# Kernel optimization log

Hardware: AMD Instinct MI355X
Metric: run time of the kernel (lower is better)

Reference implementation:

```python
import jax, jax.numpy as jnp
import numpy as np

SEQ, BATCH, HIDDEN = 2048, 2, 1024
NUM_HEADS, HEAD_DIM = 16, 64
LN_EPS = 1e-6
NEG_INF = -1e10


def setup_inputs() -> dict:
    key = jax.random.key(0)
    k1, k2, k3, k4 = jax.random.split(key, 4)
    inputs_q = jax.random.normal(k1, (SEQ, BATCH, HIDDEN), dtype=jnp.float32)
    # mask convention (TE flax): True / 1 => position is masked out
    mask = jax.random.randint(k2, (BATCH, 1, SEQ, SEQ), 0, 2).astype(bool)
    ln_scale = jnp.ones((HIDDEN,), dtype=jnp.float32)
    ln_bias = jnp.zeros((HIDDEN,), dtype=jnp.float32)
    # fused QKV kernel (embed, 3, num_heads*head_dim); query column pre-scaled
    # at init by 1/sqrt(head_dim) (scaled_query_init=True)
    w_qkv = jax.random.normal(k3, (HIDDEN, 3, NUM_HEADS * HEAD_DIM), dtype=jnp.float32) / np.sqrt(HIDDEN)
    w_qkv = w_qkv.at[:, 0, :].divide(np.sqrt(HEAD_DIM))
    w_out = jax.random.normal(k4, (NUM_HEADS * HEAD_DIM, HIDDEN), dtype=jnp.float32) / np.sqrt(NUM_HEADS * HEAD_DIM)
    return {"inputs_q": inputs_q, "mask": mask, "ln_scale": ln_scale,
            "ln_bias": ln_bias, "w_qkv": w_qkv, "w_out": w_out}


def _layernorm(x, scale, bias):
    mean = jnp.mean(x, axis=-1, keepdims=True)
    var = jnp.mean(jnp.square(x - mean), axis=-1, keepdims=True)
    return (x - mean) * jax.lax.rsqrt(var + LN_EPS) * scale + bias


def reference(inputs_q, mask, ln_scale, ln_bias, w_qkv, w_out):
    s, b, e = inputs_q.shape  # (seq, batch, hidden): transpose_batch_sequence=True
    ln_out = _layernorm(inputs_q, ln_scale, ln_bias)
    # fused QKV projection: (s,b,e) @ (e,3,H*D) -> (s,b,3,H*D)
    qkv = jnp.einsum('sbe,ekf->sbkf', ln_out, w_qkv)
    q, k, v = qkv[:, :, 0, :], qkv[:, :, 1, :], qkv[:, :, 2, :]
    q = q.reshape(s, b, NUM_HEADS, HEAD_DIM)
    k = k.reshape(s, b, NUM_HEADS, HEAD_DIM)
    v = v.reshape(s, b, NUM_HEADS, HEAD_DIM)
    # core attention, transpose_batch_sequence layout (seq, batch, h, d)
    logits = jnp.einsum('qbhd,kbhd->bhqk', q, k)
    logits = jnp.where(mask, jnp.asarray(NEG_INF, logits.dtype), logits)
    attn = jax.nn.softmax(logits, axis=-1)
    ctx = jnp.einsum('bhqk,kbhd->qbhd', attn, v).reshape(s, b, NUM_HEADS * HEAD_DIM)
    out = jnp.einsum('sbf,fe->sbe', ctx, w_out)
    return out
```

## Files before the change

kernel.cpp:

```cpp
#include <hip/hip_runtime.h>

typedef __bf16 bf16;
typedef __attribute__((ext_vector_type(8))) __bf16 bf16x8;
typedef __attribute__((ext_vector_type(4))) __bf16 bf16x4;
typedef __attribute__((ext_vector_type(4))) float f32x4;
typedef unsigned long long u64;

static constexpr int S = 2048, B = 2, H = 1024, NH = 16, HD = 64;
static constexpr int ROWS = S * B;
static constexpr int NQKV = 3 * NH * HD;
static constexpr int KBLK = 64;
static constexpr int NT = S / KBLK;
static constexpr int MW = S / 64;
static constexpr float LOG2E = 1.4426950408889634f;
static constexpr int G0_WG = (NQKV / 128) * (ROWS / 128);
static constexpr int PACK_WG = (B * S * S) / (256 * 16);

__device__ __forceinline__ int swz(int row, int col) { return col ^ ((row & 7) << 3); }

__device__ __forceinline__ void g2l16(const bf16* g, bf16* l) {
  __builtin_amdgcn_global_load_lds((const __attribute__((address_space(1))) void*)g,
                                   (__attribute__((address_space(3))) void*)l, 16, 0, 0);
}

__global__ __launch_bounds__(256) void prep_kernel(const float* __restrict__ wqkv,
                                                   const float* __restrict__ wout,
                                                   bf16* __restrict__ dqkv,
                                                   bf16* __restrict__ dout,
                                                   const float* __restrict__ x,
                                                   const float* __restrict__ sc,
                                                   const float* __restrict__ bi,
                                                   bf16* __restrict__ lnout,
                                                   const void* __restrict__ mask,
                                                   u64* __restrict__ bits) {
  __shared__ float shmem[32 * 33];
  const int bid = blockIdx.x;
  const int tid = threadIdx.x;
  if (bid < 4096) {
    const int bx = bid & 127, by = bid >> 7;
    const bool second = bx >= (NQKV / 32);
    const float* src = second ? wout : wqkv;
    bf16* dst = second ? dout : dqkv;
    const int C = second ? H : NQKV;
    const int c0 = (second ? bx - NQKV / 32 : bx) * 32, r0 = by * 32;
    const int xx = tid & 31, yy = tid >> 5;
#pragma unroll
    for (int i = 0; i < 32; i += 8)
      shmem[(yy + i) * 33 + xx] = src[(size_t)(r0 + yy + i) * C + c0 + xx];
    __syncthreads();
#pragma unroll
    for (int i = 0; i < 32; i += 8) {
      const int col = c0 + yy + i;
      const float scale = (!second && col < 1024) ? LOG2E : 1.0f;
      dst[(size_t)col * H + r0 + xx] = (bf16)(shmem[xx * 33 + yy + i] * scale);
    }
  } else if (bid < 8192) {
    const int row = bid - 4096;
    const float4 v = *(const float4*)&x[(size_t)row * H + tid * 4];
    float s = v.x + v.y + v.z + v.w;
#pragma unroll
    for (int m = 1; m < 64; m <<= 1) s += __shfl_xor(s, m);
    float* red1 = shmem;
    float* red2 = shmem + 8;
    const int w = tid >> 6, lane = tid & 63;
    if (lane == 0) red1[w] = s;
    __syncthreads();
    const float mean = (red1[0] + red1[1] + red1[2] + red1[3]) * (1.0f / H);
    const float dx = v.x - mean, dy = v.y - mean, dz = v.z - mean, dw = v.w - mean;
    float q = dx * dx + dy * dy + dz * dz + dw * dw;
#pragma unroll
    for (int m = 1; m < 64; m <<= 1) q += __shfl_xor(q, m);
    if (lane == 0) red2[w] = q;
    __syncthreads();
    const float var = (red2[0] + red2[1] + red2[2] + red2[3]) * (1.0f / H);
    const float inv = rsqrtf(var + 1e-6f);
    const float4 s4 = *(const float4*)&sc[tid * 4];
    const float4 b4 = *(const float4*)&bi[tid * 4];
    bf16x4 o;
    o[0] = (bf16)(dx * inv * s4.x + b4.x);
    o[1] = (bf16)(dy * inv * s4.y + b4.y);
    o[2] = (bf16)(dz * inv * s4.z + b4.z);
    o[3] = (bf16)(dw * inv * s4.w + b4.w);
    *(bf16x4*)&lnout[(size_t)row * H + tid * 4] = o;
  } else {
    const int p = bid - 8192;
    const size_t base = (size_t)p * 4096;
    int* det = (int*)shmem;
    if (tid == 0) det[0] = 0;
    __syncthreads();
    const uint4 wv = *(const uint4*)((const unsigned char*)mask + base + (size_t)tid * 16);
    const unsigned any3 = (wv.x | wv.y | wv.z | wv.w) & 0xFFFFFF00u;
    if (any3) atomicOr(det, 1);
    __syncthreads();
    const bool imode = (det[0] == 0);
#pragma unroll
    for (int k = 0; k < 16; ++k) {
      const size_t e = base + k * 256 + tid;
      int mv;
      if (imode) mv = ((const int*)mask)[e];
      else mv = (int)((const unsigned char*)mask)[e];
      const u64 bal = __ballot(mv != 0);
      if ((tid & 63) == 0) bits[e >> 6] = bal;
    }
  }
}

template <int EPI>
__global__ __launch_bounds__(256) void gemm128(const bf16* __restrict__ A, const bf16* __restrict__ Bt,
                                               bf16* __restrict__ qo, bf16* __restrict__ ko,
                                               bf16* __restrict__ vo, float* __restrict__ out) {
  constexpr int K = 1024;
  constexpr int NKT = K / 64;
  __shared__ __align__(16) bf16 As[2][128][64];
  __shared__ __align__(16) bf16 Bs[2][128][64];
  int lin, NX, total;
  if (EPI == 0) {
    lin = blockIdx.x;
    NX = NQKV / 128; total = G0_WG;
  } else {
    lin = blockIdx.y * gridDim.x + blockIdx.x;
    NX = gridDim.x; total = gridDim.x * gridDim.y;
  }
  const int cpx = total >> 3;
  const int work = (lin & 7) * cpx + (lin >> 3);
  const int bm = (work / NX) * 128, bn = (work % NX) * 128;
  const bool isV = (EPI == 0) && (bn >= 2048);
  const int tid = threadIdx.x;
  const int wave = tid >> 6, lane = tid & 63;
  const int wm = (wave >> 1) * 64, wn = (wave & 1) * 64;
  const int g = lane >> 4, l15 = lane & 15;
  const int lr = lane >> 3;
  const int lc = 8 * ((lane & 7) ^ lr);
  const bf16* Ab = &A[(size_t)bm * K];
  const bf16* Bb = &Bt[(size_t)bn * K];

  f32x4 acc[4][4] = {};
#pragma unroll
  for (int p = 0; p < 4; ++p) {
    const int r0 = wave * 32 + p * 8;
    g2l16(&Ab[(size_t)(r0 + lr) * K + lc], &As[0][r0][0]);
    g2l16(&Bb[(size_t)(r0 + lr) * K + lc], &Bs[0][r0][0]);
  }
  __syncthreads();

  for (int kt = 0; kt < NKT; ++kt) {
    const int cur = kt & 1;
    if (kt + 1 < NKT) {
      const int ko2 = (kt + 1) * 64;
#pragma unroll
      for (int p = 0; p < 4; ++p) {
        const int r0 = wave * 32 + p * 8;
        g2l16(&Ab[(size_t)(r0 + lr) * K + ko2 + lc], &As[cur ^ 1][r0][0]);
        g2l16(&Bb[(size_t)(r0 + lr) * K + ko2 + lc], &Bs[cur ^ 1][r0][0]);
      }
    }
#pragma unroll
    for (int ks = 0; ks < 2; ++ks) {
      bf16x8 af[4], bb[4];
#pragma unroll
      for (int i = 0; i < 4; ++i) af[i] = *(const bf16x8*)&As[cur][wm + i * 16 + l15][swz(l15, ks * 32 + g * 8)];
#pragma unroll
      for (int j = 0; j < 4; ++j) bb[j] = *(const bf16x8*)&Bs[cur][wn + j * 16 + l15][swz(l15, ks * 32 + g * 8)];
      __builtin_amdgcn_s_setprio(1);
      if (isV) {
#pragma unroll
        for (int i = 0; i < 4; ++i)
#pragma unroll
          for (int j = 0; j < 4; ++j)
            acc[i][j] = __builtin_amdgcn_mfma_f32_16x16x32_bf16(bb[j], af[i], acc[i][j], 0, 0, 0);
      } else {
#pragma unroll
        for (int i = 0; i < 4; ++i)
#pragma unroll
          for (int j = 0; j < 4; ++j)
            acc[i][j] = __builtin_amdgcn_mfma_f32_16x16x32_bf16(af[i], bb[j], acc[i][j], 0, 0, 0);
      }
      __builtin_amdgcn_s_setprio(0);
    }
    __syncthreads();
  }
#pragma unroll
  for (int i = 0; i < 4; ++i) {
#pragma unroll
    for (int j = 0; j < 4; ++j) {
#pragma unroll
      for (int r = 0; r < 4; ++r) {
        const float val = acc[i][j][r];
        if (isV) {
          const int row = bm + wm + i * 16 + l15;
          const int col = bn + wn + j * 16 + g * 4 + r;
          const int f = col & 1023;
          const int h = f >> 6, d = f & 63;
          const int sdx = row >> 1, b = row & 1;
          vo[(((size_t)b * NH + h) * HD + d) * S + sdx] = (bf16)val;
        } else if (EPI == 0) {
          const int row = bm + wm + i * 16 + g * 4 + r;
          const int col = bn + wn + j * 16 + l15;
          const int kk = col >> 10, f = col & 1023;
          const int h = f >> 6, d = f & 63;
          const int sdx = row >> 1, b = row & 1;
          const size_t head = (size_t)b * NH + h;
          if (kk == 0)
            qo[(head * S + sdx) * HD + d] = (bf16)val;
          else
            ko[(head * S + sdx) * HD + d] = (bf16)val;
        } else {
          const int row = bm + wm + i * 16 + g * 4 + r;
          const int col = bn + wn + j * 16 + l15;
          out[(size_t)row * H + col] = val;
        }
      }
    }
  }
}

__global__ __launch_bounds__(512, 4) void attn_kernel(const bf16* __restrict__ Qb, const bf16* __restrict__ Kb,
                                                      const bf16* __restrict__ Vt, const u64* __restrict__ mbits,
                                                      bf16* __restrict__ ctx) {
  __shared__ __align__(16) bf16 Ks[2][64][64];
  __shared__ __align__(16) bf16 Vs[2][64][64];
  __shared__ __align__(16) bf16 P[8][16][64];
  const int lin = blockIdx.y * 16 + blockIdx.x;
  const int work = ((lin & 7) << 6) | (lin >> 3);
  const int bh = work >> 4, qb = work & 15;
  const int b = bh >> 4, h = bh & 15;
  const int tid = threadIdx.x, w = tid >> 6, lane = tid & 63;
  const int g = lane >> 4, c = lane & 15;
  const int q0 = qb * 128 + w * 16;
  const size_t head = (size_t)b * NH + h;
  const bf16* Qh = Qb + head * S * HD;
  const bf16* Kh = Kb + head * S * HD;
  const bf16* Vh = Vt + head * HD * S;

  const int srow = w * 8 + (lane >> 3);
  const int scol = 8 * ((lane & 7) ^ (lane >> 3));

  bf16x8 aq[2];
#pragma unroll
  for (int ks = 0; ks < 2; ++ks)
    aq[ks] = *(const bf16x8*)&Qh[(size_t)(q0 + c) * HD + ks * 32 + g * 8];

  f32x4 o[4] = {};
  float lsum = 0.f;

  g2l16(&Kh[(size_t)srow * HD + scol], &Ks[0][w * 8][0]);
  g2l16(&Vh[(size_t)srow * S + scol], &Vs[0][w * 8][0]);
  __syncthreads();

  for (int t = 0; t < NT; ++t) {
    const int cur = t & 1;
    if (t + 1 < NT) {
      const int kt1 = (t + 1) * KBLK;
      g2l16(&Kh[(size_t)(kt1 + srow) * HD + scol], &Ks[cur ^ 1][w * 8][0]);
      g2l16(&Vh[(size_t)srow * S + kt1 + scol], &Vs[cur ^ 1][w * 8][0]);
    }
    f32x4 sv[4] = {};
#pragma unroll
    for (int ks = 0; ks < 2; ++ks) {
      bf16x8 bk[4];
#pragma unroll
      for (int j = 0; j < 4; ++j)
        bk[j] = *(const bf16x8*)&Ks[cur][j * 16 + c][swz(c, ks * 32 + g * 8)];
      __builtin_amdgcn_s_setprio(1);
#pragma unroll
      for (int j = 0; j < 4; ++j)
        sv[j] = __builtin_amdgcn_mfma_f32_16x16x32_bf16(bk[j], aq[ks], sv[j], 0, 0, 0);
      __builtin_amdgcn_s_setprio(0);
    }
    {
      const u64 mb = mbits[((size_t)b * S + q0 + c) * MW + t];
      const unsigned mlo = (unsigned)mb, mhi = (unsigned)(mb >> 32);
      f32x4 acc4 = {0.f, 0.f, 0.f, 0.f};
#pragma unroll
      for (int j = 0; j < 4; ++j) {
        const unsigned word = (j < 2) ? mlo : mhi;
        const unsigned sub = word >> (((j & 1) << 4) + (g << 2));
        bf16x4 pk;
#pragma unroll
        for (int r = 0; r < 4; ++r) {
          float e = __builtin_amdgcn_exp2f(sv[j][r]);
          if ((sub >> r) & 1u) e = 0.f;
          pk[r] = (bf16)e;
          acc4[r] += e;
        }
        *(bf16x4*)&P[w][c][(j * 16 + g * 4) ^ ((c & 7) << 3)] = pk;
      }
      lsum += (acc4[0] + acc4[1]) + (acc4[2] + acc4[3]);
    }
    __threadfence_block();
#pragma unroll
    for (int ks = 0; ks < 2; ++ks) {
      const bf16x8 pa = *(const bf16x8*)&P[w][c][(ks * 32 + g * 8) ^ ((c & 7) << 3)];
      bf16x8 bv[4];
#pragma unroll
      for (int j = 0; j < 4; ++j)
        bv[j] = *(const bf16x8*)&Vs[cur][j * 16 + c][swz(c, ks * 32 + g * 8)];
      __builtin_amdgcn_s_setprio(1);
#pragma unroll
      for (int j = 0; j < 4; ++j)
        o[j] = __builtin_amdgcn_mfma_f32_16x16x32_bf16(pa, bv[j], o[j], 0, 0, 0);
      __builtin_amdgcn_s_setprio(0);
    }
    __syncthreads();
  }
  lsum += __shfl_xor(lsum, 16);
  lsum += __shfl_xor(lsum, 32);
#pragma unroll
  for (int r = 0; r < 4; ++r) {
    const float denom = __shfl(lsum, g * 4 + r);
    const float inv = 1.0f / denom;
    const int qrow = q0 + g * 4 + r;
#pragma unroll
    for (int j = 0; j < 4; ++j)
      ctx[((size_t)qrow * B + b) * H + h * HD + j * 16 + c] = (bf16)(o[j][r] * inv);
  }
}

extern "C" void kernel_launch(void* const* d_in, const int* in_sizes, int n_in,
                              void* d_out, int out_size, void* d_ws, size_t ws_size,
                              hipStream_t stream) {
  const float* x = (const float*)d_in[0];
  const void* mask = d_in[1];
  const float* ln_scale = (const float*)d_in[2];
  const float* ln_bias = (const float*)d_in[3];
  const float* w_qkv = (const float*)d_in[4];
  const float* w_out = (const float*)d_in[5];
  float* out = (float*)d_out;

  char* ws = (char*)d_ws;
  size_t off = 0;
  u64* mbits = (u64*)(ws + off); off += (size_t)B * S * (S / 8);
  bf16* lnb   = (bf16*)(ws + off); off += (size_t)ROWS * H * 2;
  bf16* wqkvt = (bf16*)(ws + off); off += (size_t)NQKV * H * 2;
  bf16* woutt = (bf16*)(ws + off); off += (size_t)H * H * 2;
  bf16* Qb    = (bf16*)(ws + off); off += (size_t)B * NH * S * HD * 2;
  bf16* Kb    = (bf16*)(ws + off); off += (size_t)B * NH * S * HD * 2;
  bf16* Vt    = (bf16*)(ws + off); off += (size_t)B * NH * S * HD * 2;
  bf16* ctx   = (bf16*)(ws + off); off += (size_t)ROWS * H * 2;

  prep_kernel<<<8192 + PACK_WG, 256, 0, stream>>>(w_qkv, w_out, wqkvt, woutt, x, ln_scale, ln_bias, lnb,
                                                  mask, mbits);
  gemm128<0><<<G0_WG, 256, 0, stream>>>(lnb, wqkvt, Qb, Kb, Vt, nullptr);
  attn_kernel<<<dim3(S / 128, B * NH), 512, 0, stream>>>(Qb, Kb, Vt, mbits, ctx);
  gemm128<1><<<dim3(H / 128, ROWS / 128), 256, 0, stream>>>(ctx, woutt, nullptr, nullptr, nullptr, out);
}
```

Measured before the change: 142.2 us.

## Give each attention wave two query tiles to reuse K/V fragments

The attention block shrinks from 8 waves of 16 query rows each to 4 waves of 32 query rows each. Every K and V fragment read from LDS now feeds two MFMAs, which halves LDS read traffic per query row, and each thread issues twice as many async global-to-LDS copies. In exchange, register pressure rises from the doubled accumulators and scores, there are fewer waves per block to hide latency, and the launch bound drops to 256 threads with 2 blocks per multiprocessor.

```diff
diff --git a/kernel.cpp b/kernel.cpp
--- a/kernel.cpp
+++ b/kernel.cpp
@@ -214,47 +214,53 @@
   }
 }
 
-__global__ __launch_bounds__(512, 4) void attn_kernel(const bf16* __restrict__ Qb, const bf16* __restrict__ Kb,
+__global__ __launch_bounds__(256, 2) void attn_kernel(const bf16* __restrict__ Qb, const bf16* __restrict__ Kb,
                                                       const bf16* __restrict__ Vt, const u64* __restrict__ mbits,
                                                       bf16* __restrict__ ctx) {
   __shared__ __align__(16) bf16 Ks[2][64][64];
   __shared__ __align__(16) bf16 Vs[2][64][64];
-  __shared__ __align__(16) bf16 P[8][16][64];
+  __shared__ __align__(16) bf16 P[4][2][16][64];
   const int lin = blockIdx.y * 16 + blockIdx.x;
   const int work = ((lin & 7) << 6) | (lin >> 3);
   const int bh = work >> 4, qb = work & 15;
   const int b = bh >> 4, h = bh & 15;
   const int tid = threadIdx.x, w = tid >> 6, lane = tid & 63;
   const int g = lane >> 4, c = lane & 15;
-  const int q0 = qb * 128 + w * 16;
+  const int q0 = qb * 128 + w * 32;
   const size_t head = (size_t)b * NH + h;
   const bf16* Qh = Qb + head * S * HD;
   const bf16* Kh = Kb + head * S * HD;
   const bf16* Vh = Vt + head * HD * S;
 
-  const int srow = w * 8 + (lane >> 3);
+  const int sra = w * 16 + (lane >> 3);
   const int scol = 8 * ((lane & 7) ^ (lane >> 3));
 
-  bf16x8 aq[2];
-#pragma unroll
-  for (int ks = 0; ks < 2; ++ks)
-    aq[ks] = *(const bf16x8*)&Qh[(size_t)(q0 + c) * HD + ks * 32 + g * 8];
-
-  f32x4 o[4] = {};
-  float lsum = 0.f;
-
-  g2l16(&Kh[(size_t)srow * HD + scol], &Ks[0][w * 8][0]);
-  g2l16(&Vh[(size_t)srow * S + scol], &Vs[0][w * 8][0]);
+  bf16x8 aq[2][2];
+#pragma unroll
+  for (int i = 0; i < 2; ++i)
+#pragma unroll
+    for (int ks = 0; ks < 2; ++ks)
+      aq[i][ks] = *(const bf16x8*)&Qh[(size_t)(q0 + i * 16 + c) * HD + ks * 32 + g * 8];
+
+  f32x4 o[2][4] = {};
+  float lsum[2] = {0.f, 0.f};
+
+  g2l16(&Kh[(size_t)sra * HD + scol], &Ks[0][w * 16][0]);
+  g2l16(&Kh[(size_t)(sra + 8) * HD + scol], &Ks[0][w * 16 + 8][0]);
+  g2l16(&Vh[(size_t)sra * S + scol], &Vs[0][w * 16][0]);
+  g2l16(&Vh[(size_t)(sra + 8) * S + scol], &Vs[0][w * 16 + 8][0]);
   __syncthreads();
 
   for (int t = 0; t < NT; ++t) {
     const int cur = t & 1;
     if (t + 1 < NT) {
       const int kt1 = (t + 1) * KBLK;
-      g2l16(&Kh[(size_t)(kt1 + srow) * HD + scol], &Ks[cur ^ 1][w * 8][0]);
-      g2l16(&Vh[(size_t)srow * S + kt1 + scol], &Vs[cur ^ 1][w * 8][0]);
-    }
-    f32x4 sv[4] = {};
+      g2l16(&Kh[(size_t)(kt1 + sra) * HD + scol], &Ks[cur ^ 1][w * 16][0]);
+      g2l16(&Kh[(size_t)(kt1 + sra + 8) * HD + scol], &Ks[cur ^ 1][w * 16 + 8][0]);
+      g2l16(&Vh[(size_t)sra * S + kt1 + scol], &Vs[cur ^ 1][w * 16][0]);
+      g2l16(&Vh[(size_t)(sra + 8) * S + kt1 + scol], &Vs[cur ^ 1][w * 16 + 8][0]);
+    }
+    f32x4 sv[2][4] = {};
 #pragma unroll
     for (int ks = 0; ks < 2; ++ks) {
       bf16x8 bk[4];
@@ -263,12 +269,15 @@
         bk[j] = *(const bf16x8*)&Ks[cur][j * 16 + c][swz(c, ks * 32 + g * 8)];
       __builtin_amdgcn_s_setprio(1);
 #pragma unroll
-      for (int j = 0; j < 4; ++j)
-        sv[j] = __builtin_amdgcn_mfma_f32_16x16x32_bf16(bk[j], aq[ks], sv[j], 0, 0, 0);
+      for (int i = 0; i < 2; ++i)
+#pragma unroll
+        for (int j = 0; j < 4; ++j)
+          sv[i][j] = __builtin_amdgcn_mfma_f32_16x16x32_bf16(bk[j], aq[i][ks], sv[i][j], 0, 0, 0);
       __builtin_amdgcn_s_setprio(0);
     }
-    {
-      const u64 mb = mbits[((size_t)b * S + q0 + c) * MW + t];
+#pragma unroll
+    for (int i = 0; i < 2; ++i) {
+      const u64 mb = mbits[((size_t)b * S + q0 + i * 16 + c) * MW + t];
       const unsigned mlo = (unsigned)mb, mhi = (unsigned)(mb >> 32);
       f32x4 acc4 = {0.f, 0.f, 0.f, 0.f};
 #pragma unroll
@@ -278,41 +287,48 @@
         bf16x4 pk;
 #pragma unroll
         for (int r = 0; r < 4; ++r) {
-          float e = __builtin_amdgcn_exp2f(sv[j][r]);
+          float e = __builtin_amdgcn_exp2f(sv[i][j][r]);
           if ((sub >> r) & 1u) e = 0.f;
           pk[r] = (bf16)e;
           acc4[r] += e;
         }
-        *(bf16x4*)&P[w][c][(j * 16 + g * 4) ^ ((c & 7) << 3)] = pk;
-      }
-      lsum += (acc4[0] + acc4[1]) + (acc4[2] + acc4[3]);
+        *(bf16x4*)&P[w][i][c][(j * 16 + g * 4) ^ ((c & 7) << 3)] = pk;
+      }
+      lsum[i] += (acc4[0] + acc4[1]) + (acc4[2] + acc4[3]);
     }
     __threadfence_block();
 #pragma unroll
     for (int ks = 0; ks < 2; ++ks) {
-      const bf16x8 pa = *(const bf16x8*)&P[w][c][(ks * 32 + g * 8) ^ ((c & 7) << 3)];
       bf16x8 bv[4];
 #pragma unroll
       for (int j = 0; j < 4; ++j)
         bv[j] = *(const bf16x8*)&Vs[cur][j * 16 + c][swz(c, ks * 32 + g * 8)];
+      const bf16x8 pa0 = *(const bf16x8*)&P[w][0][c][(ks * 32 + g * 8) ^ ((c & 7) << 3)];
+      const bf16x8 pa1 = *(const bf16x8*)&P[w][1][c][(ks * 32 + g * 8) ^ ((c & 7) << 3)];
       __builtin_amdgcn_s_setprio(1);
 #pragma unroll
+      for (int j = 0; j < 4; ++j) {
+        o[0][j] = __builtin_amdgcn_mfma_f32_16x16x32_bf16(pa0, bv[j], o[0][j], 0, 0, 0);
+        o[1][j] = __builtin_amdgcn_mfma_f32_16x16x32_bf16(pa1, bv[j], o[1][j], 0, 0, 0);
+      }
+      __builtin_amdgcn_s_setprio(0);
+    }
+    __syncthreads();
+  }
+#pragma unroll
+  for (int i = 0; i < 2; ++i) {
+    float ls = lsum[i];
+    ls += __shfl_xor(ls, 16);
+    ls += __shfl_xor(ls, 32);
+#pragma unroll
+    for (int r = 0; r < 4; ++r) {
+      const float denom = __shfl(ls, g * 4 + r);
+      const float inv = 1.0f / denom;
+      const int qrow = q0 + i * 16 + g * 4 + r;
+#pragma unroll
       for (int j = 0; j < 4; ++j)
-        o[j] = __builtin_amdgcn_mfma_f32_16x16x32_bf16(pa, bv[j], o[j], 0, 0, 0);
-      __builtin_amdgcn_s_setprio(0);
-    }
-    __syncthreads();
-  }
-  lsum += __shfl_xor(lsum, 16);
-  lsum += __shfl_xor(lsum, 32);
-#pragma unroll
-  for (int r = 0; r < 4; ++r) {
-    const float denom = __shfl(lsum, g * 4 + r);
-    const float inv = 1.0f / denom;
-    const int qrow = q0 + g * 4 + r;
-#pragma unroll
-    for (int j = 0; j < 4; ++j)
-      ctx[((size_t)qrow * B + b) * H + h * HD + j * 16 + c] = (bf16)(o[j][r] * inv);
+        ctx[((size_t)qrow * B + b) * H + h * HD + j * 16 + c] = (bf16)(o[i][j][r] * inv);
+    }
   }
 }
 
@@ -341,6 +357,6 @@
   prep_kernel<<<8192 + PACK_WG, 256, 0, stream>>>(w_qkv, w_out, wqkvt, woutt, x, ln_scale, ln_bias, lnb,
                                                   mask, mbits);
   gemm128<0><<<G0_WG, 256, 0, stream>>>(lnb, wqkvt, Qb, Kb, Vt, nullptr);
-  attn_kernel<<<dim3(S / 128, B * NH), 512, 0, stream>>>(Qb, Kb, Vt, mbits, ctx);
+  attn_kernel<<<dim3(S / 128, B * NH), 256, 0, stream>>>(Qb, Kb, Vt, mbits, ctx);
   gemm128<1><<<dim3(H / 128, ROWS / 128), 256, 0, stream>>>(ctx, woutt, nullptr, nullptr, nullptr, out);
 }
```

New measurement: 147.4 us. 3.7% more time.
